# Kernel optimization log

Hardware: AMD Instinct MI355X
Metric: run time of the kernel (lower is better)

The kernel has to match this reference:

```python
import jax, jax.numpy as jnp
import numpy as np

N, E, R, B, IN, H, OUT, P = 20000, 320000, 8, 8, 128, 256, 128, 100000
LN_EPS = 1e-5


def _xavier(key, shape):
    fan_in, fan_out = shape[-2], shape[-1]
    lim = float(np.sqrt(6.0 / (fan_in + fan_out)))
    return jax.random.uniform(key, shape, jnp.float32, -lim, lim)


def setup_inputs() -> dict:
    key = jax.random.key(0)
    ks = iter(jax.random.split(key, 64))
    inp = {}
    inp['x'] = jax.random.normal(next(ks), (N, IN), jnp.float32)
    inp['edge_index'] = jax.random.randint(next(ks), (2, E), 0, N, jnp.int32)
    inp['edge_type'] = jax.random.randint(next(ks), (E,), 0, R, jnp.int32)
    inp['gene_pairs'] = jax.random.randint(next(ks), (2, P), 0, N, jnp.int32)
    dims = [(IN, H), (H, H), (H, H), (H, OUT)]  # per-layer (in_ch, out_ch)
    for i, (ic, oc) in enumerate(dims):
        inp[f'basis{i}'] = _xavier(next(ks), (B, ic, oc))
        inp[f'att{i}'] = _xavier(next(ks), (R, B))
        inp[f'root{i}'] = _xavier(next(ks), (ic, oc))
        inp[f'relatt{i}'] = jnp.ones((R,), jnp.float32)
        inp[f'g{i}'] = jnp.ones((oc,), jnp.float32)
        inp[f'b{i}'] = jnp.zeros((oc,), jnp.float32)
    inp['res0'] = _xavier(next(ks), (IN, H))   # in_ch != out_ch at layer 0
    inp['res3'] = _xavier(next(ks), (H, OUT))  # and at layer 3
    # decoder: 3*OUT -> H -> H//2 -> H//4 -> 1
    ddims = [(3 * OUT, H), (H, H // 2), (H // 2, H // 4), (H // 4, 1)]
    for i, (ic, oc) in enumerate(ddims):
        inp[f'dW{i}'] = _xavier(next(ks), (ic, oc))
        inp[f'db{i}'] = jnp.zeros((oc,), jnp.float32)
        if i < 3:
            inp[f'dg{i}'] = jnp.ones((oc,), jnp.float32)
            inp[f'dbb{i}'] = jnp.zeros((oc,), jnp.float32)
    return inp


def _ln(h, g, b):
    m = h.mean(-1, keepdims=True)
    v = ((h - m) ** 2).mean(-1, keepdims=True)
    return (h - m) * jax.lax.rsqrt(v + LN_EPS) * g + b


def _conv(x, src, dst, et, basis, att, root_w, rel_att):
    # W_r = sum_b att[r,b] * B_b ; message = a_{r(e)} * x_src @ W_{r(e)}
    # Since the message is linear, aggregate x_src per (dst, relation) first
    # (segment_sum), then apply the R small GEMMs once - same math, no [E,in,out].
    n, d = x.shape
    weight = jnp.einsum('rb,bio->rio', att, basis)          # [R,in,out]
    a = jax.nn.softmax(rel_att)                              # [R]
    seg = dst.astype(jnp.int32) * R + et.astype(jnp.int32)   # [(node,rel)] segment ids
    agg = jax.ops.segment_sum(x[src], seg, num_segments=n * R).reshape(n, R, d)
    out = jnp.einsum('nri,rio->no', agg, weight * a[:, None, None])
    return out + x @ root_w


def reference(x, edge_index, edge_type, gene_pairs,
              basis0, att0, root0, relatt0, g0, b0, res0,
              basis1, att1, root1, relatt1, g1, b1,
              basis2, att2, root2, relatt2, g2, b2,
              basis3, att3, root3, relatt3, g3, b3, res3,
              dW0, db0, dg0, dbb0, dW1, db1, dg1, dbb1,
              dW2, db2, dg2, dbb2, dW3, db3):
    src, dst = edge_index[0], edge_index[1]
    layers = [
        (basis0, att0, root0, relatt0, g0, b0, res0),
        (basis1, att1, root1, relatt1, g1, b1, None),
        (basis2, att2, root2, relatt2, g2, b2, None),
        (basis3, att3, root3, relatt3, g3, b3, res3),
    ]
    h = x
    for i, (bs, at, rt, ra, g, b, res) in enumerate(layers):
        h_in = h
        h = _conv(h, src, dst, edge_type, bs, at, rt, ra)
        h = _ln(h, g, b)
        h = h + (h_in @ res if res is not None else h_in)
        if i < len(layers) - 1:
            h = jax.nn.gelu(h, approximate=False)
    z = h  # [N, OUT]
    zi, zj = z[gene_pairs[0]], z[gene_pairs[1]]
    pe = jnp.concatenate([zi + zj, zi * zj, jnp.abs(zi - zj)], axis=-1)
    d = jax.nn.gelu(_ln(pe @ dW0 + db0, dg0, dbb0), approximate=False)
    d = jax.nn.gelu(_ln(d @ dW1 + db1, dg1, dbb1), approximate=False)
    d = jax.nn.gelu(_ln(d @ dW2 + db2, dg2, dbb2), approximate=False)
    logits = (d @ dW3 + db3).squeeze(-1)  # [P]
    return logits, z
```

## Files before the change

### kernel.cpp

```cpp
#include <hip/hip_runtime.h>
#include <hip/hip_bf16.h>
#include <math.h>
#include <cstddef>
#include <stdint.h>

#define NN 20000
#define EE 320000
#define RR 8
#define PP 100000
#define NR (NN * RR)

typedef __hip_bfloat16 bf16;
typedef __attribute__((ext_vector_type(8))) short short8;
typedef __attribute__((ext_vector_type(4))) short short4v;
typedef __attribute__((ext_vector_type(4))) float floatx4;
typedef __attribute__((ext_vector_type(4))) int intx4;

__device__ __forceinline__ float b2f(bf16 v) { return __bfloat162float(v); }
__device__ __forceinline__ bf16 f2b(float v) { return __float2bfloat16(v); }
__device__ __forceinline__ float bits2f(unsigned short u) {
  unsigned int i = ((unsigned int)u) << 16; float f; __builtin_memcpy(&f, &i, 4); return f;
}
__device__ __forceinline__ short f2bits(float f) {
  bf16 h = __float2bfloat16(f); short s; __builtin_memcpy(&s, &h, 2); return s;
}
__device__ __forceinline__ float gelu_f(float x) {
  float t = x * (0.7978845608f + 0.0356774081f * x * x);
  float s = exp2f(-2.885390082f * t);
  return x * __builtin_amdgcn_rcpf(1.f + s);
}
__device__ __forceinline__ void async_copy16(void* lds, const void* g) {
  __builtin_amdgcn_global_load_lds((const __attribute__((address_space(1))) void*)g,
                                   (__attribute__((address_space(3))) void*)lds, 16, 0, 0);
}
__device__ __forceinline__ const short8* frag_at(const bf16* base, int row, int q) {
  return (const short8*)(base + row * 64 + (((q) ^ (row & 7)) << 3));
}
__device__ __forceinline__ const short8* frag256(const bf16* base, int row, int col64, int q) {
  return (const short8*)(base + row * 256 + col64 + (((q) ^ (row & 7)) << 3));
}
__device__ __forceinline__ int idx128(int row, int qg) {
  return row * 128 + ((qg >> 3) << 6) + (((qg & 7) ^ (row & 7)) << 3);
}

__global__ void hist_k(const int* __restrict__ dst, const int* __restrict__ et,
                       int* __restrict__ counts) {
  int e = blockIdx.x * 256 + threadIdx.x;
  if (e >= EE) return;
  atomicAdd(&counts[dst[e] * RR + et[e]], 1);
}

__global__ void scan1_k(const int* __restrict__ counts, int* __restrict__ prefix,
                        int* __restrict__ bsums) {
  __shared__ int tmp[256];
  int i = blockIdx.x * 256 + threadIdx.x;
  int v = counts[i];
  tmp[threadIdx.x] = v; __syncthreads();
  for (int off = 1; off < 256; off <<= 1) {
    int x = (threadIdx.x >= off) ? tmp[threadIdx.x - off] : 0;
    __syncthreads();
    tmp[threadIdx.x] += x;
    __syncthreads();
  }
  prefix[i] = tmp[threadIdx.x] - v;
  if (threadIdx.x == 255) bsums[blockIdx.x] = tmp[255];
}

__global__ void scan2_k(int* __restrict__ bsums, int nb) {
  __shared__ int tmp[256];
  __shared__ int carry;
  if (threadIdx.x == 0) carry = 0;
  __syncthreads();
  for (int base = 0; base < nb; base += 256) {
    int i = base + threadIdx.x;
    int v = (i < nb) ? bsums[i] : 0;
    tmp[threadIdx.x] = v; __syncthreads();
    for (int off = 1; off < 256; off <<= 1) {
      int x = (threadIdx.x >= off) ? tmp[threadIdx.x - off] : 0;
      __syncthreads();
      tmp[threadIdx.x] += x;
      __syncthreads();
    }
    int c = carry;
    if (i < nb) bsums[i] = c + tmp[threadIdx.x] - v;
    __syncthreads();
    if (threadIdx.x == 255) carry = c + tmp[255];
    __syncthreads();
  }
}

__global__ void scan3_k(int* __restrict__ prefix, const int* __restrict__ bsums) {
  int i = blockIdx.x * 256 + threadIdx.x;
  prefix[i] += bsums[blockIdx.x];
}

__global__ void scatter_k(const int* __restrict__ src, const int* __restrict__ dst,
                          const int* __restrict__ et, const int* __restrict__ segstart,
                          int* __restrict__ cursor, int* __restrict__ ssrc) {
  int e = blockIdx.x * 256 + threadIdx.x;
  if (e >= EE) return;
  int s = dst[e] * RR + et[e];
  int pos = atomicAdd(&cursor[s], 1);
  ssrc[segstart[s] + pos] = src[e];
}

__global__ void cvt_bf16_k(const float* __restrict__ in, bf16* __restrict__ out, int n) {
  int i = blockIdx.x * 256 + threadIdx.x;
  if (i < n) out[i] = f2b(in[i]);
}

__global__ void softmax4_k(const float* r0, const float* r1, const float* r2,
                           const float* r3, float* __restrict__ a) {
  if (threadIdx.x == 0) {
    const float* rs[4] = {r0, r1, r2, r3};
    for (int l = 0; l < 4; ++l) {
      float mx = -1e30f;
      for (int i = 0; i < RR; ++i) mx = fmaxf(mx, rs[l][i]);
      float e[RR]; float s = 0.f;
      for (int i = 0; i < RR; ++i) { e[i] = expf(rs[l][i] - mx); s += e[i]; }
      for (int i = 0; i < RR; ++i) a[l * RR + i] = e[i] / s;
    }
  }
}

__global__ void transpose_k(const float* __restrict__ in, bf16* __restrict__ out,
                            int rows, int cols) {
  int idx = blockIdx.x * 256 + threadIdx.x;
  if (idx >= rows * cols) return;
  int r = idx / cols, c = idx - r * cols;
  out[(size_t)c * rows + r] = f2b(in[idx]);
}

__global__ void transpose_pe_k(const float* __restrict__ wb, const float* __restrict__ wc,
                               bf16* __restrict__ wpe) {
  int idx = blockIdx.x * 256 + threadIdx.x;
  if (idx >= 128 * 256) return;
  int k = idx >> 8;
  int o = idx & 255;
  wpe[(size_t)o * 256 + k] = f2b(wb[idx]);
  wpe[(size_t)o * 256 + 128 + k] = f2b(wc[idx]);
}

__global__ void prep_w_k(const float* __restrict__ basis, const float* __restrict__ att,
                         const float* __restrict__ root, const float* __restrict__ a,
                         bf16* __restrict__ Wt, int ic, int icsh, int oc, int ocsh) {
  int idx = blockIdx.x * 256 + threadIdx.x;
  int cols = 9 * ic;
  if (idx >= cols * oc) return;
  int o = idx & (oc - 1);
  int col = idx >> ocsh;
  int r = col >> icsh;
  int k = col & (ic - 1);
  float val;
  if (r < RR) {
    float acc = 0.f;
    for (int bb = 0; bb < RR; ++bb)
      acc += att[r * RR + bb] * basis[((size_t)bb * ic + k) * oc + o];
    val = a[r] * acc;
  } else {
    val = root[(size_t)k * oc + o];
  }
  Wt[(size_t)o * cols + col] = f2b(val);
}

__global__ __launch_bounds__(256) void aggregate_k(
    const bf16* __restrict__ h, const int* __restrict__ segstart,
    const int* __restrict__ counts, const int* __restrict__ ssrc,
    bf16* __restrict__ agg, int ic, int tpnsh) {
  int tpn = 1 << tpnsh;
  int npb = 256 >> tpnsh;
  int local = threadIdx.x >> tpnsh;
  int n = blockIdx.x * npb + local;
  if (n >= NN) return;
  int cbase = (threadIdx.x & (tpn - 1)) * 8;
  size_t rowoff = (size_t)n * (9 * ic);
  const bf16* hc = h + cbase;

  intx4 stv0 = *(const intx4*)(segstart + n * RR);
  intx4 stv1 = *(const intx4*)(segstart + n * RR + 4);
  intx4 ctv0 = *(const intx4*)(counts + n * RR);
  intx4 ctv1 = *(const intx4*)(counts + n * RR + 4);
  int sts[8] = {stv0[0], stv0[1], stv0[2], stv0[3], stv1[0], stv1[1], stv1[2], stv1[3]};
  int cts[8] = {ctv0[0], ctv0[1], ctv0[2], ctv0[3], ctv1[0], ctv1[1], ctv1[2], ctv1[3]};

#pragma unroll
  for (int rp = 0; rp < 4; ++rp) {
    const int stA = sts[rp],     cA = cts[rp];
    const int stB = sts[rp + 4], cB = cts[rp + 4];
    float aA[8] = {0.f, 0.f, 0.f, 0.f, 0.f, 0.f, 0.f, 0.f};
    float aB[8] = {0.f, 0.f, 0.f, 0.f, 0.f, 0.f, 0.f, 0.f};
    int iA = 0, iB = 0;
    while (iA + 2 <= cA && iB + 2 <= cB) {
      int sA0 = ssrc[stA + iA], sA1 = ssrc[stA + iA + 1];
      int sB0 = ssrc[stB + iB], sB1 = ssrc[stB + iB + 1];
      short8 vA0 = *(const short8*)(hc + (size_t)sA0 * ic);
      short8 vA1 = *(const short8*)(hc + (size_t)sA1 * ic);
      short8 vB0 = *(const short8*)(hc + (size_t)sB0 * ic);
      short8 vB1 = *(const short8*)(hc + (size_t)sB1 * ic);
#pragma unroll
      for (int j = 0; j < 8; ++j) {
        aA[j] += bits2f((unsigned short)vA0[j]) + bits2f((unsigned short)vA1[j]);
        aB[j] += bits2f((unsigned short)vB0[j]) + bits2f((unsigned short)vB1[j]);
      }
      iA += 2; iB += 2;
    }
    for (; iA + 2 <= cA; iA += 2) {
      int s0 = ssrc[stA + iA], s1 = ssrc[stA + iA + 1];
      short8 v0 = *(const short8*)(hc + (size_t)s0 * ic);
      short8 v1 = *(const short8*)(hc + (size_t)s1 * ic);
#pragma unroll
      for (int j = 0; j < 8; ++j)
        aA[j] += bits2f((unsigned short)v0[j]) + bits2f((unsigned short)v1[j]);
    }
    if (iA < cA) {
      int s0 = ssrc[stA + iA];
      short8 v0 = *(const short8*)(hc + (size_t)s0 * ic);
#pragma unroll
      for (int j = 0; j < 8; ++j) aA[j] += bits2f((unsigned short)v0[j]);
    }
    for (; iB + 2 <= cB; iB += 2) {
      int s0 = ssrc[stB + iB], s1 = ssrc[stB + iB + 1];
      short8 v0 = *(const short8*)(hc + (size_t)s0 * ic);
      short8 v1 = *(const short8*)(hc + (size_t)s1 * ic);
#pragma unroll
      for (int j = 0; j < 8; ++j)
        aB[j] += bits2f((unsigned short)v0[j]) + bits2f((unsigned short)v1[j]);
    }
    if (iB < cB) {
      int s0 = ssrc[stB + iB];
      short8 v0 = *(const short8*)(hc + (size_t)s0 * ic);
#pragma unroll
      for (int j = 0; j < 8; ++j) aB[j] += bits2f((unsigned short)v0[j]);
    }
    short8 oA, oB;
#pragma unroll
    for (int j = 0; j < 8; ++j) { oA[j] = f2bits(aA[j]); oB[j] = f2bits(aB[j]); }
    *(short8*)(agg + rowoff + rp * ic + cbase) = oA;
    *(short8*)(agg + rowoff + (rp + 4) * ic + cbase) = oB;
  }
  *(short8*)(agg + rowoff + 8 * ic + cbase) =
      *(const short8*)(h + (size_t)n * ic + cbase);
}

__global__ __launch_bounds__(256) void gemm_f32_k(
    const bf16* __restrict__ A, const bf16* __restrict__ Wt,
    float* __restrict__ Cf, int M, int N, int K, int nb) {
  const int bid = blockIdx.x;
  const int xcd = bid & 7;
  const int slot = bid >> 3;
  const int gidx = slot / nb;
  const int member = slot - gidx * nb;
  const int mb = (M + 127) >> 7;
  const int m = gidx * 8 + xcd;
  if (m >= mb) return;
  const int m0 = m * 128;
  const int n0 = member * 64;

  __shared__ __align__(16) bf16 As[128 * 64];
  __shared__ __align__(16) bf16 Ws[64 * 64];
  const int tid = threadIdx.x;
  const int wave = tid >> 6, lane = tid & 63;
  const int quad = lane >> 4, l16 = lane & 15;
  const int wm = (wave >> 1) * 64, wn = (wave & 1) * 32;
  floatx4 acc[4][2];
#pragma unroll
  for (int i = 0; i < 4; ++i)
#pragma unroll
    for (int j = 0; j < 2; ++j) acc[i][j] = (floatx4){0.f, 0.f, 0.f, 0.f};

  for (int k0 = 0; k0 < K; k0 += 64) {
#pragma unroll
    for (int q = 0; q < 4; ++q) {
      int c0 = (wave * 4 + q) * 1024;
      int row = (c0 >> 7) + (lane >> 3);
      int grow = m0 + row; if (grow >= M) grow = M - 1;
      int ch = (lane & 7) ^ (row & 7);
      async_copy16((char*)As + c0, A + (size_t)grow * K + k0 + ch * 8);
    }
#pragma unroll
    for (int q = 0; q < 2; ++q) {
      int c0 = (wave * 2 + q) * 1024;
      int row = (c0 >> 7) + (lane >> 3);
      int ch = (lane & 7) ^ (row & 7);
      async_copy16((char*)Ws + c0, Wt + (size_t)(n0 + row) * K + k0 + ch * 8);
    }
    __syncthreads();
#pragma unroll
    for (int kk = 0; kk < 64; kk += 32) {
      int qb = (kk >> 3) + quad;
      short8 b0 = *frag_at(Ws, wn + l16, qb);
      short8 b1 = *frag_at(Ws, wn + 16 + l16, qb);
#pragma unroll
      for (int i = 0; i < 4; ++i) {
        short8 a = *frag_at(As, wm + i * 16 + l16, qb);
        acc[i][0] = __builtin_amdgcn_mfma_f32_16x16x32_bf16(a, b0, acc[i][0], 0, 0, 0);
        acc[i][1] = __builtin_amdgcn_mfma_f32_16x16x32_bf16(a, b1, acc[i][1], 0, 0, 0);
      }
    }
    __syncthreads();
  }
#pragma unroll
  for (int i = 0; i < 4; ++i)
#pragma unroll
    for (int j = 0; j < 2; ++j)
#pragma unroll
      for (int r = 0; r < 4; ++r) {
        int row = m0 + wm + i * 16 + quad * 4 + r;
        int col = n0 + wn + j * 16 + l16;
        if (row < M) Cf[(size_t)row * N + col] = acc[i][j][r];
      }
}

__global__ __launch_bounds__(256) void gemm_plain_k(
    const bf16* __restrict__ A, const bf16* __restrict__ Wt,
    bf16* __restrict__ Cb, int M, int N, int K) {
  __shared__ __align__(16) bf16 As[64 * 64];
  __shared__ __align__(16) bf16 Ws[64 * 64];
  const int m0 = blockIdx.y * 64;
  const int n0 = blockIdx.x * 64;
  const int tid = threadIdx.x;
  const int wave = tid >> 6, lane = tid & 63;
  const int quad = lane >> 4, l16 = lane & 15;
  const int wm = (wave >> 1) * 32, wn = (wave & 1) * 32;
  floatx4 acc00 = {0.f, 0.f, 0.f, 0.f};
  floatx4 acc01 = acc00, acc10 = acc00, acc11 = acc00;

  for (int k0 = 0; k0 < K; k0 += 64) {
#pragma unroll
    for (int q = 0; q < 2; ++q) {
      int c0 = (wave * 2 + q) * 1024;
      int row = (c0 >> 7) + (lane >> 3);
      int grow = m0 + row; if (grow >= M) grow = M - 1;
      int ch = (lane & 7) ^ (row & 7);
      async_copy16((char*)As + c0, A + (size_t)grow * K + k0 + ch * 8);
    }
#pragma unroll
    for (int q = 0; q < 2; ++q) {
      int c0 = (wave * 2 + q) * 1024;
      int row = (c0 >> 7) + (lane >> 3);
      int ch = (lane & 7) ^ (row & 7);
      async_copy16((char*)Ws + c0, Wt + (size_t)(n0 + row) * K + k0 + ch * 8);
    }
    __syncthreads();
#pragma unroll
    for (int kk = 0; kk < 64; kk += 32) {
      int qb = (kk >> 3) + quad;
      short8 a0 = *frag_at(As, wm + l16, qb);
      short8 a1 = *frag_at(As, wm + 16 + l16, qb);
      short8 b0 = *frag_at(Ws, wn + l16, qb);
      short8 b1 = *frag_at(Ws, wn + 16 + l16, qb);
      acc00 = __builtin_amdgcn_mfma_f32_16x16x32_bf16(a0, b0, acc00, 0, 0, 0);
      acc01 = __builtin_amdgcn_mfma_f32_16x16x32_bf16(a0, b1, acc01, 0, 0, 0);
      acc10 = __builtin_amdgcn_mfma_f32_16x16x32_bf16(a1, b0, acc10, 0, 0, 0);
      acc11 = __builtin_amdgcn_mfma_f32_16x16x32_bf16(a1, b1, acc11, 0, 0, 0);
    }
    __syncthreads();
  }
  floatx4 accs[2][2] = {{acc00, acc01}, {acc10, acc11}};
#pragma unroll
  for (int i = 0; i < 2; ++i)
#pragma unroll
    for (int j = 0; j < 2; ++j)
#pragma unroll
      for (int r = 0; r < 4; ++r) {
        int row = m0 + wm + i * 16 + quad * 4 + r;
        int col = n0 + wn + j * 16 + l16;
        if (row < M) Cb[(size_t)row * N + col] = f2b(accs[i][j][r]);
      }
}

__global__ __launch_bounds__(256) void ln_conv_k(
    const float* __restrict__ conv, const bf16* __restrict__ res,
    const float* __restrict__ g, const float* __restrict__ b,
    bf16* __restrict__ out, float* __restrict__ zout, int oc, int do_gelu) {
  int wave = threadIdx.x >> 6, lane = threadIdx.x & 63;
  int row = blockIdx.x * 4 + wave;
  if (row >= NN) return;
  int ne = oc >> 6;
  float v[4];
  float s = 0.f, s2 = 0.f;
  for (int i = 0; i < ne; ++i) {
    v[i] = conv[(size_t)row * oc + i * 64 + lane];
    s += v[i]; s2 += v[i] * v[i];
  }
  for (int off = 32; off; off >>= 1) { s += __shfl_xor(s, off); s2 += __shfl_xor(s2, off); }
  float m = s / oc;
  float var = s2 / oc - m * m;
  float rs = rsqrtf(var + 1e-5f);
  for (int i = 0; i < ne; ++i) {
    int c = i * 64 + lane;
    float y = (v[i] - m) * rs * g[c] + b[c];
    y += b2f(res[(size_t)row * oc + c]);
    if (zout) zout[(size_t)row * oc + c] = y;
    if (do_gelu) y = gelu_f(y);
    out[(size_t)row * oc + c] = f2b(y);
  }
}

__global__ __launch_bounds__(256) void gemm_pe_k(
    const bf16* __restrict__ z, const int* __restrict__ pairs,
    const bf16* __restrict__ WPE,
    bf16* __restrict__ P0) {
  const int bid = blockIdx.x;
  const int xcd = bid & 7;
  const int slot = bid >> 3;
  const int mb = (PP + 127) >> 7;
  const int m = slot * 8 + xcd;
  if (m >= mb) return;
  const int m0 = m * 128;

  __shared__ __align__(16) bf16 PEs[128 * 128];
  const int tid = threadIdx.x;
  const int wave = tid >> 6, lane = tid & 63;
  const int quad = lane >> 4, l16 = lane & 15;
  const int wm = (wave >> 1) * 64;
  const int wn = (wave & 1) * 128;

  const int prow = tid >> 1;
  const int h = tid & 1;
  int pp = m0 + prow; if (pp >= PP) pp = PP - 1;
  const bf16* zi = z + (size_t)pairs[pp] * 128;
  const bf16* zj = z + (size_t)pairs[PP + pp] * 128;

  floatx4 acc[4][8];
#pragma unroll
  for (int i = 0; i < 4; ++i)
#pragma unroll
    for (int j = 0; j < 8; ++j) acc[i][j] = (floatx4){0.f, 0.f, 0.f, 0.f};

#pragma unroll
  for (int kwi = 0; kwi < 2; ++kwi) {
    const int kw = kwi * 64;
    short8 va[4], vb[4];
#pragma unroll
    for (int c8 = 0; c8 < 4; ++c8) {
      va[c8] = *(const short8*)(zi + kw + h * 32 + c8 * 8);
      vb[c8] = *(const short8*)(zj + kw + h * 32 + c8 * 8);
    }
    if (kwi) __syncthreads();
#pragma unroll
    for (int c8 = 0; c8 < 4; ++c8) {
      short8 op, od;
#pragma unroll
      for (int jj = 0; jj < 8; ++jj) {
        float fa = bits2f((unsigned short)va[c8][jj]);
        float fb = bits2f((unsigned short)vb[c8][jj]);
        op[jj] = f2bits(fa * fb);
        od[jj] = f2bits(fabsf(fa - fb));
      }
      *(short8*)(PEs + idx128(prow, h * 4 + c8)) = op;
      *(short8*)(PEs + idx128(prow, 8 + h * 4 + c8)) = od;
    }
    __syncthreads();
#pragma unroll
    for (int kk = 0; kk < 4; ++kk) {
      const int c = kk * 4 + quad;
      const int gk = (kk < 2) ? (kw + c * 8) : (128 + kw + (c - 8) * 8);
      short8 bf[8];
#pragma unroll
      for (int j = 0; j < 8; ++j)
        bf[j] = *(const short8*)(WPE + (size_t)(wn + j * 16 + l16) * 256 + gk);
      short8 af[4];
#pragma unroll
      for (int i = 0; i < 4; ++i)
        af[i] = *(const short8*)(PEs + idx128(wm + i * 16 + l16, c));
#pragma unroll
      for (int i = 0; i < 4; ++i)
#pragma unroll
        for (int j = 0; j < 8; ++j)
          acc[i][j] = __builtin_amdgcn_mfma_f32_16x16x32_bf16(af[i], bf[j], acc[i][j], 0, 0, 0);
    }
  }

#pragma unroll
  for (int i = 0; i < 4; ++i)
#pragma unroll
    for (int j = 0; j < 8; ++j)
#pragma unroll
      for (int r = 0; r < 4; ++r) {
        int row = m0 + wm + i * 16 + quad * 4 + r;
        int col = wn + j * 16 + l16;
        if (row < PP) P0[(size_t)row * 256 + col] = f2b(acc[i][j][r]);
      }
}

__global__ __launch_bounds__(256) void ln_d0_k(bf16* __restrict__ D0,
                                               const int* __restrict__ pairs,
                                               const bf16* __restrict__ ZA,
                                               const float* __restrict__ db0,
                                               const float* __restrict__ g,
                                               const float* __restrict__ b) {
  const int wave = threadIdx.x >> 6, lane = threadIdx.x & 63;
  const int row = blockIdx.x * 8 + wave * 2 + (lane >> 5);
  const int cb = (lane & 31) * 8;
  int gi = pairs[row], gj = pairs[PP + row];
  bf16* p = D0 + (size_t)row * 256 + cb;
  short8 xv = *(const short8*)p;
  short8 av = *(const short8*)(ZA + (size_t)gi * 256 + cb);
  short8 bv = *(const short8*)(ZA + (size_t)gj * 256 + cb);
  float v[8];
  float s = 0.f, s2 = 0.f;
#pragma unroll
  for (int k = 0; k < 8; ++k) {
    v[k] = bits2f((unsigned short)xv[k]) + bits2f((unsigned short)av[k]) +
           bits2f((unsigned short)bv[k]) + db0[cb + k];
    s += v[k]; s2 += v[k] * v[k];
  }
  for (int off = 16; off; off >>= 1) { s += __shfl_xor(s, off); s2 += __shfl_xor(s2, off); }
  float m = s / 256.f;
  float var = s2 / 256.f - m * m;
  float rs = rsqrtf(var + 1e-5f);
  short8 ov;
#pragma unroll
  for (int k = 0; k < 8; ++k) {
    float y = (v[k] - m) * rs * g[cb + k] + b[cb + k];
    ov[k] = f2bits(gelu_f(y));
  }
  *(short8*)p = ov;
}

__global__ __launch_bounds__(256) void lngemm1_k(
    const bf16* __restrict__ D0, const bf16* __restrict__ W1t,
    const float* __restrict__ bias, bf16* __restrict__ P1, int M) {
  __shared__ __align__(16) bf16 As[64 * 256];
  __shared__ __align__(16) bf16 Ws[128 * 64];
  const int tid = threadIdx.x;
  const int wave = tid >> 6, lane = tid & 63;
  const int quad = lane >> 4, l16 = lane & 15;
  const int wr = (wave >> 1) * 32;
  const int wc = (wave & 1) * 64;
  const int m0 = blockIdx.x * 64;

  {
    const int srow = tid >> 2;
    const int q4 = tid & 3;
    int grow = m0 + srow; if (grow >= M) grow = M - 1;
    const bf16* src = D0 + (size_t)grow * 256 + q4 * 64;
#pragma unroll
    for (int c8 = 0; c8 < 8; ++c8) {
      short8 o = *(const short8*)(src + c8 * 8);
      *(short8*)(As + srow * 256 + q4 * 64 + ((c8 ^ (srow & 7)) << 3)) = o;
    }
  }

  floatx4 acc[2][4];
#pragma unroll
  for (int i = 0; i < 2; ++i)
#pragma unroll
    for (int j = 0; j < 4; ++j) acc[i][j] = (floatx4){0.f, 0.f, 0.f, 0.f};

  for (int kc = 0; kc < 4; ++kc) {
#pragma unroll
    for (int q = 0; q < 4; ++q) {
      int c0 = q * 4096 + wave * 1024;
      int row = (c0 >> 7) + (lane >> 3);
      int ch = (lane & 7) ^ (row & 7);
      async_copy16((char*)Ws + c0, W1t + (size_t)row * 256 + kc * 64 + ch * 8);
    }
    __syncthreads();
#pragma unroll
    for (int kk = 0; kk < 64; kk += 32) {
      int qb = (kk >> 3) + quad;
      short8 a0 = *frag256(As, wr + l16, kc * 64, qb);
      short8 a1 = *frag256(As, wr + 16 + l16, kc * 64, qb);
#pragma unroll
      for (int j = 0; j < 4; ++j) {
        short8 bb = *frag_at(Ws, wc + j * 16 + l16, qb);
        acc[0][j] = __builtin_amdgcn_mfma_f32_16x16x32_bf16(a0, bb, acc[0][j], 0, 0, 0);
        acc[1][j] = __builtin_amdgcn_mfma_f32_16x16x32_bf16(a1, bb, acc[1][j], 0, 0, 0);
      }
    }
    __syncthreads();
  }

#pragma unroll
  for (int i = 0; i < 2; ++i)
#pragma unroll
    for (int r = 0; r < 4; ++r) {
      int row = wr + i * 16 + quad * 4 + r;
      int grow = m0 + row;
      if (grow >= M) continue;
#pragma unroll
      for (int j = 0; j < 4; ++j) {
        int col = wc + j * 16 + l16;
        P1[(size_t)grow * 128 + col] = f2b(acc[i][j][r] + bias[col]);
      }
    }
}

__global__ __launch_bounds__(256) void lngemm2_k(
    const bf16* __restrict__ P1, const bf16* __restrict__ W2t,
    const float* __restrict__ g, const float* __restrict__ b,
    const float* __restrict__ bias, bf16* __restrict__ P2, int M) {
  __shared__ __align__(16) bf16 As[64 * 128];
  __shared__ __align__(16) bf16 Ws[64 * 64];
  const int tid = threadIdx.x;
  const int wave = tid >> 6, lane = tid & 63;
  const int quad = lane >> 4, l16 = lane & 15;
  const int m0 = blockIdx.x * 64;

  {
    const int srow = tid >> 2;
    const int q4 = tid & 3;
    int grow = m0 + srow; if (grow >= M) grow = M - 1;
    const bf16* src = P1 + (size_t)grow * 128 + q4 * 32;
    float v[32];
    float s = 0.f, s2 = 0.f;
#pragma unroll
    for (int c8 = 0; c8 < 4; ++c8) {
      short8 x = *(const short8*)(src + c8 * 8);
#pragma unroll
      for (int jj = 0; jj < 8; ++jj) {
        float f = bits2f((unsigned short)x[jj]);
        v[c8 * 8 + jj] = f; s += f; s2 += f * f;
      }
    }
    s += __shfl_xor(s, 1); s2 += __shfl_xor(s2, 1);
    s += __shfl_xor(s, 2); s2 += __shfl_xor(s2, 2);
    float mean = s / 128.f;
    float var = s2 / 128.f - mean * mean;
    float rs = rsqrtf(var + 1e-5f);
#pragma unroll
    for (int c8 = 0; c8 < 4; ++c8) {
      short8 o;
#pragma unroll
      for (int jj = 0; jj < 8; ++jj) {
        int col = q4 * 32 + c8 * 8 + jj;
        float y = (v[c8 * 8 + jj] - mean) * rs * g[col] + b[col];
        o[jj] = f2bits(gelu_f(y));
      }
      *(short8*)(As + idx128(srow, q4 * 4 + c8)) = o;
    }
  }

  floatx4 acc[4];
#pragma unroll
  for (int j = 0; j < 4; ++j) acc[j] = (floatx4){0.f, 0.f, 0.f, 0.f};

  for (int kc = 0; kc < 2; ++kc) {
#pragma unroll
    for (int q = 0; q < 2; ++q) {
      int c0 = q * 4096 + wave * 1024;
      int row = (c0 >> 7) + (lane >> 3);
      int ch = (lane & 7) ^ (row & 7);
      async_copy16((char*)Ws + c0, W2t + (size_t)row * 128 + kc * 64 + ch * 8);
    }
    __syncthreads();
#pragma unroll
    for (int kk = 0; kk < 64; kk += 32) {
      int qb = (kk >> 3) + quad;
      short8 a = *(const short8*)(As + idx128(wave * 16 + l16, kc * 8 + qb));
#pragma unroll
      for (int j = 0; j < 4; ++j) {
        short8 bb = *frag_at(Ws, j * 16 + l16, qb);
        acc[j] = __builtin_amdgcn_mfma_f32_16x16x32_bf16(a, bb, acc[j], 0, 0, 0);
      }
    }
    __syncthreads();
  }

#pragma unroll
  for (int r = 0; r < 4; ++r) {
    int row = wave * 16 + quad * 4 + r;
    int grow = m0 + row;
    if (grow >= M) continue;
#pragma unroll
    for (int j = 0; j < 4; ++j) {
      int col = j * 16 + l16;
      P2[(size_t)grow * 64 + col] = f2b(acc[j][r] + bias[col]);
    }
  }
}

__global__ __launch_bounds__(256) void logits_k(const bf16* __restrict__ P2,
                                                const float* __restrict__ g,
                                                const float* __restrict__ b,
                                                const float* __restrict__ w3,
                                                const float* __restrict__ b3,
                                                float* __restrict__ out) {
  int wave = threadIdx.x >> 6, lane = threadIdx.x & 63;
  int p = blockIdx.x * 4 + wave;
  if (p >= PP) return;
  float v = b2f(P2[(size_t)p * 64 + lane]);
  float s = v, s2 = v * v;
  for (int off = 32; off; off >>= 1) { s += __shfl_xor(s, off); s2 += __shfl_xor(s2, off); }
  float m = s / 64.f;
  float var = s2 / 64.f - m * m;
  float rs = rsqrtf(var + 1e-5f);
  float y = gelu_f((v - m) * rs * g[lane] + b[lane]);
  float t = y * w3[lane];
  for (int off = 32; off; off >>= 1) t += __shfl_xor(t, off);
  if (lane == 0) out[p] = t + b3[0];
}

extern "C" void kernel_launch(void* const* d_in, const int* in_sizes, int n_in,
                              void* d_out, int out_size, void* d_ws, size_t ws_size,
                              hipStream_t stream) {
  auto cdiv = [](int a, int b) { return (a + b - 1) / b; };

  const float* x = (const float*)d_in[0];
  const int* ei = (const int*)d_in[1];
  const int* et = (const int*)d_in[2];
  const int* gp = (const int*)d_in[3];
  const float *basis[4], *att[4], *root[4], *relatt[4], *gln[4], *bln[4];
  for (int l = 0; l < 4; ++l) {
    basis[l]  = (const float*)d_in[4 + 6 * l];
    att[l]    = (const float*)d_in[5 + 6 * l];
    root[l]   = (const float*)d_in[6 + 6 * l];
    relatt[l] = (const float*)d_in[7 + 6 * l];
    gln[l]    = (const float*)d_in[8 + 6 * l];
    bln[l]    = (const float*)d_in[9 + 6 * l];
  }
  const float* res0 = (const float*)d_in[28];
  const float* res3 = (const float*)d_in[29];
  const float* dW0 = (const float*)d_in[30]; const float* db0 = (const float*)d_in[31];
  const float* dg0 = (const float*)d_in[32]; const float* dbb0 = (const float*)d_in[33];
  const float* dW1 = (const float*)d_in[34]; const float* db1 = (const float*)d_in[35];
  const float* dg1 = (const float*)d_in[36]; const float* dbb1 = (const float*)d_in[37];
  const float* dW2 = (const float*)d_in[38]; const float* db2 = (const float*)d_in[39];
  const float* dg2 = (const float*)d_in[40]; const float* dbb2 = (const float*)d_in[41];
  const float* dW3 = (const float*)d_in[42]; const float* db3 = (const float*)d_in[43];

  char* base = (char*)d_ws;
  size_t off = 0;
  auto alloc = [&](size_t bytes) -> char* {
    char* p = base + off;
    off += (bytes + 255) & ~(size_t)255;
    return p;
  };
  bf16* X16 = (bf16*)alloc((size_t)NN * 128 * 2);
  bf16* HA  = (bf16*)alloc((size_t)NN * 256 * 2);
  bf16* HB  = (bf16*)alloc((size_t)NN * 256 * 2);
  bf16* RESB = (bf16*)alloc((size_t)NN * 256 * 2);
  bf16* ZA   = (bf16*)alloc((size_t)NN * 256 * 2);
  float* CONV = (float*)alloc((size_t)NN * 256 * 4);
  bf16* WT    = (bf16*)alloc((size_t)589824 * 2);
  bf16* RES0T = (bf16*)alloc((size_t)32768 * 2);
  bf16* RES3T = (bf16*)alloc((size_t)32768 * 2);
  bf16* WAT   = (bf16*)alloc((size_t)32768 * 2);
  bf16* WPE   = (bf16*)alloc((size_t)65536 * 2);
  bf16* DW1T  = (bf16*)alloc((size_t)32768 * 2);
  bf16* DW2T  = (bf16*)alloc((size_t)8192 * 2);
  float* ASOFT = (float*)alloc(32 * 4);
  int* COUNTS = (int*)alloc((size_t)NR * 4);
  int* SEG    = (int*)alloc((size_t)NR * 4);
  int* CUR    = (int*)alloc((size_t)NR * 4);
  int* BS     = (int*)alloc(1024 * 4);
  int* SSRC   = (int*)alloc((size_t)EE * 4);
  char* BIG = alloc(93000000);
  bf16* AGG = (bf16*)BIG;
  bf16* P0  = (bf16*)BIG;
  bf16* P1  = (bf16*)alloc((size_t)PP * 128 * 2);
  bf16* P2  = (bf16*)alloc((size_t)PP * 64 * 2);
  (void)ws_size; (void)in_sizes; (void)n_in; (void)out_size;

  float* out_logits = (float*)d_out;
  float* out_z = (float*)d_out + PP;

  hipMemsetAsync(COUNTS, 0, (size_t)NR * 4, stream);
  hipMemsetAsync(CUR, 0, (size_t)NR * 4, stream);
  hist_k<<<cdiv(EE, 256), 256, 0, stream>>>(ei + EE, et, COUNTS);
  scan1_k<<<NR / 256, 256, 0, stream>>>(COUNTS, SEG, BS);
  scan2_k<<<1, 256, 0, stream>>>(BS, NR / 256);
  scan3_k<<<NR / 256, 256, 0, stream>>>(SEG, BS);
  scatter_k<<<cdiv(EE, 256), 256, 0, stream>>>(ei, ei + EE, et, SEG, CUR, SSRC);

  cvt_bf16_k<<<cdiv(NN * 128, 256), 256, 0, stream>>>(x, X16, NN * 128);
  softmax4_k<<<1, 64, 0, stream>>>(relatt[0], relatt[1], relatt[2], relatt[3], ASOFT);
  transpose_k<<<cdiv(128 * 256, 256), 256, 0, stream>>>(res0, RES0T, 128, 256);
  transpose_k<<<cdiv(256 * 128, 256), 256, 0, stream>>>(res3, RES3T, 256, 128);
  transpose_k<<<cdiv(128 * 256, 256), 256, 0, stream>>>(dW0, WAT, 128, 256);
  transpose_pe_k<<<cdiv(128 * 256, 256), 256, 0, stream>>>(dW0 + 128 * 256, dW0 + 256 * 256, WPE);
  transpose_k<<<cdiv(256 * 128, 256), 256, 0, stream>>>(dW1, DW1T, 256, 128);
  transpose_k<<<cdiv(128 * 64, 256), 256, 0, stream>>>(dW2, DW2T, 128, 64);

  const int mb = cdiv(NN, 128);
  const int swzP4 = 8 * cdiv(mb, 8) * 4;
  const int swzP2 = 8 * cdiv(mb, 8) * 2;

  prep_w_k<<<cdiv(9 * 128 * 256, 256), 256, 0, stream>>>(basis[0], att[0], root[0], ASOFT + 0, WT, 128, 7, 256, 8);
  aggregate_k<<<cdiv(NN, 16), 256, 0, stream>>>(X16, SEG, COUNTS, SSRC, AGG, 128, 4);
  gemm_plain_k<<<dim3(4, cdiv(NN, 64)), 256, 0, stream>>>(X16, RES0T, RESB, NN, 256, 128);
  gemm_f32_k<<<swzP4, 256, 0, stream>>>(AGG, WT, CONV, NN, 256, 1152, 4);
  ln_conv_k<<<cdiv(NN, 4), 256, 0, stream>>>(CONV, RESB, gln[0], bln[0], HA, nullptr, 256, 1);

  prep_w_k<<<cdiv(9 * 256 * 256, 256), 256, 0, stream>>>(basis[1], att[1], root[1], ASOFT + 8, WT, 256, 8, 256, 8);
  aggregate_k<<<cdiv(NN, 8), 256, 0, stream>>>(HA, SEG, COUNTS, SSRC, AGG, 256, 5);
  gemm_f32_k<<<swzP4, 256, 0, stream>>>(AGG, WT, CONV, NN, 256, 2304, 4);
  ln_conv_k<<<cdiv(NN, 4), 256, 0, stream>>>(CONV, HA, gln[1], bln[1], HB, nullptr, 256, 1);

  prep_w_k<<<cdiv(9 * 256 * 256, 256), 256, 0, stream>>>(basis[2], att[2], root[2], ASOFT + 16, WT, 256, 8, 256, 8);
  aggregate_k<<<cdiv(NN, 8), 256, 0, stream>>>(HB, SEG, COUNTS, SSRC, AGG, 256, 5);
  gemm_f32_k<<<swzP4, 256, 0, stream>>>(AGG, WT, CONV, NN, 256, 2304, 4);
  ln_conv_k<<<cdiv(NN, 4), 256, 0, stream>>>(CONV, HB, gln[2], bln[2], HA, nullptr, 256, 1);

  prep_w_k<<<cdiv(9 * 256 * 128, 256), 256, 0, stream>>>(basis[3], att[3], root[3], ASOFT + 24, WT, 256, 8, 128, 7);
  aggregate_k<<<cdiv(NN, 8), 256, 0, stream>>>(HA, SEG, COUNTS, SSRC, AGG, 256, 5);
  gemm_plain_k<<<dim3(2, cdiv(NN, 64)), 256, 0, stream>>>(HA, RES3T, RESB, NN, 128, 256);
  gemm_f32_k<<<swzP2, 256, 0, stream>>>(AGG, WT, CONV, NN, 128, 2304, 2);
  ln_conv_k<<<cdiv(NN, 4), 256, 0, stream>>>(CONV, RESB, gln[3], bln[3], HB, out_z, 128, 0);

  gemm_plain_k<<<dim3(4, cdiv(NN, 64)), 256, 0, stream>>>(HB, WAT, ZA, NN, 256, 128);
  const int pb = cdiv(PP, 128);
  const int swzPE = 8 * cdiv(pb, 8);
  gemm_pe_k<<<swzPE, 256, 0, stream>>>(HB, gp, WPE, P0);
  ln_d0_k<<<cdiv(PP, 8), 256, 0, stream>>>(P0, gp, ZA, db0, dg0, dbb0);
  lngemm1_k<<<cdiv(PP, 64), 256, 0, stream>>>(P0, DW1T, db1, P1, PP);
  lngemm2_k<<<cdiv(PP, 64), 256, 0, stream>>>(P1, DW2T, dg1, dbb1, db2, P2, PP);
  logits_k<<<cdiv(PP, 4), 256, 0, stream>>>(P2, dg2, dbb2, dW3, db3, out_logits);
}
```

Baseline: 727.7 us.

## Split pair-embedding GEMM into N-column tiles and stage weights in LDS

The pair-feature GEMM kernel now splits the 256 output columns into four 64-column blocks, so there are four times as many workgroups. Each block's weight slice is copied asynchronously into a swizzled shared-memory tile instead of being read from global memory per wave. This cuts per-thread accumulator registers and aims for better occupancy and weight reuse. The cost is that every column block recomputes the gathered z_i*z_j and |z_i-z_j| features, so the gather and elementwise work is done four times.

```diff
diff --git a/kernel.cpp b/kernel.cpp
--- a/kernel.cpp
+++ b/kernel.cpp
@@ -404,17 +404,20 @@
   const int bid = blockIdx.x;
   const int xcd = bid & 7;
   const int slot = bid >> 3;
+  const int gidx = slot >> 2;
+  const int member = slot & 3;
   const int mb = (PP + 127) >> 7;
-  const int m = slot * 8 + xcd;
+  const int m = gidx * 8 + xcd;
   if (m >= mb) return;
   const int m0 = m * 128;
+  const int n0 = member * 64;
 
   __shared__ __align__(16) bf16 PEs[128 * 128];
+  __shared__ __align__(16) bf16 Ws[64 * 128];
   const int tid = threadIdx.x;
   const int wave = tid >> 6, lane = tid & 63;
   const int quad = lane >> 4, l16 = lane & 15;
-  const int wm = (wave >> 1) * 64;
-  const int wn = (wave & 1) * 128;
+  const int wm = (wave >> 1) * 64, wn = (wave & 1) * 32;
 
   const int prow = tid >> 1;
   const int h = tid & 1;
@@ -422,11 +425,11 @@
   const bf16* zi = z + (size_t)pairs[pp] * 128;
   const bf16* zj = z + (size_t)pairs[PP + pp] * 128;
 
-  floatx4 acc[4][8];
+  floatx4 acc[4][2];
 #pragma unroll
   for (int i = 0; i < 4; ++i)
 #pragma unroll
-    for (int j = 0; j < 8; ++j) acc[i][j] = (floatx4){0.f, 0.f, 0.f, 0.f};
+    for (int j = 0; j < 2; ++j) acc[i][j] = (floatx4){0.f, 0.f, 0.f, 0.f};
 
 #pragma unroll
   for (int kwi = 0; kwi < 2; ++kwi) {
@@ -438,6 +441,14 @@
       vb[c8] = *(const short8*)(zj + kw + h * 32 + c8 * 8);
     }
     if (kwi) __syncthreads();
+#pragma unroll
+    for (int q = 0; q < 4; ++q) {
+      int c0 = (wave * 4 + q) * 1024;
+      int r = (c0 >> 8) + (lane >> 4);
+      int s = lane & 15;
+      async_copy16((char*)Ws + c0,
+                   WPE + (size_t)(n0 + r) * 256 + ((s >> 3) << 7) + kw + (((s & 7) ^ (r & 7)) << 3));
+    }
 #pragma unroll
     for (int c8 = 0; c8 < 4; ++c8) {
       short8 op, od;
@@ -453,33 +464,27 @@
     }
     __syncthreads();
 #pragma unroll
-    for (int kk = 0; kk < 4; ++kk) {
-      const int c = kk * 4 + quad;
-      const int gk = (kk < 2) ? (kw + c * 8) : (128 + kw + (c - 8) * 8);
-      short8 bf[8];
-#pragma unroll
-      for (int j = 0; j < 8; ++j)
-        bf[j] = *(const short8*)(WPE + (size_t)(wn + j * 16 + l16) * 256 + gk);
-      short8 af[4];
-#pragma unroll
-      for (int i = 0; i < 4; ++i)
-        af[i] = *(const short8*)(PEs + idx128(wm + i * 16 + l16, c));
-#pragma unroll
-      for (int i = 0; i < 4; ++i)
-#pragma unroll
-        for (int j = 0; j < 8; ++j)
-          acc[i][j] = __builtin_amdgcn_mfma_f32_16x16x32_bf16(af[i], bf[j], acc[i][j], 0, 0, 0);
+    for (int ks = 0; ks < 4; ++ks) {
+      const int qg = ks * 4 + quad;
+      short8 b0 = *(const short8*)(Ws + idx128(wn + l16, qg));
+      short8 b1 = *(const short8*)(Ws + idx128(wn + 16 + l16, qg));
+#pragma unroll
+      for (int i = 0; i < 4; ++i) {
+        short8 a = *(const short8*)(PEs + idx128(wm + i * 16 + l16, qg));
+        acc[i][0] = __builtin_amdgcn_mfma_f32_16x16x32_bf16(a, b0, acc[i][0], 0, 0, 0);
+        acc[i][1] = __builtin_amdgcn_mfma_f32_16x16x32_bf16(a, b1, acc[i][1], 0, 0, 0);
+      }
     }
   }
 
 #pragma unroll
   for (int i = 0; i < 4; ++i)
 #pragma unroll
-    for (int j = 0; j < 8; ++j)
+    for (int j = 0; j < 2; ++j)
 #pragma unroll
       for (int r = 0; r < 4; ++r) {
         int row = m0 + wm + i * 16 + quad * 4 + r;
-        int col = wn + j * 16 + l16;
+        int col = n0 + wn + j * 16 + l16;
         if (row < PP) P0[(size_t)row * 256 + col] = f2b(acc[i][j][r]);
       }
 }
@@ -802,7 +807,7 @@
 
   gemm_plain_k<<<dim3(4, cdiv(NN, 64)), 256, 0, stream>>>(HB, WAT, ZA, NN, 256, 128);
   const int pb = cdiv(PP, 128);
-  const int swzPE = 8 * cdiv(pb, 8);
+  const int swzPE = 8 * cdiv(pb, 8) * 4;
   gemm_pe_k<<<swzPE, 256, 0, stream>>>(HB, gp, WPE, P0);
   ln_d0_k<<<cdiv(PP, 8), 256, 0, stream>>>(P0, gp, ZA, db0, dg0, dbb0);
   lngemm1_k<<<cdiv(PP, 64), 256, 0, stream>>>(P0, DW1T, db1, P1, PP);
```

Measured after the change: 698.9 us. 1.04x faster.
